# Kernel tuning notes

Hardware: AMD Instinct MI355X
Metric: run time of the kernel (lower is better)

## Reference

```python
import jax, jax.numpy as jnp
import numpy as np

N = 4096
D = 1024  # hidden_size == att_size


def setup_inputs() -> dict:
    key = jax.random.key(0)
    ks = jax.random.split(key, 10)
    s = 0.02
    return {
        "q": jax.random.normal(ks[0], (N, D), jnp.float32),
        "k": jax.random.normal(ks[1], (N, D), jnp.float32),
        "v": jax.random.normal(ks[2], (N, D), jnp.float32),
        "bias": jax.random.normal(ks[3], (N, N), jnp.float32) * s,
        "Wq": jax.random.normal(ks[4], (D, D), jnp.float32) * s,
        "bq": jnp.zeros((D,), jnp.float32),
        "Wk": jax.random.normal(ks[5], (D, D), jnp.float32) * s,
        "bk": jnp.zeros((D,), jnp.float32),
        "Wv": jax.random.normal(ks[6], (D, D), jnp.float32) * s,
        "bv": jnp.zeros((D,), jnp.float32),
    }


def reference(q, k, v, bias, Wq, bq, Wk, bk, Wv, bv):
    d = q.shape[-1]
    scale = d ** (-0.5)
    # QKV projections (nn.Linear: x @ W.T + b)
    qp = (q @ Wq.T + bq) * scale          # [N, D]
    kp = k @ Wk.T + bk                    # [N, D]
    vp = v @ Wv.T + bv                    # [N, D]
    # full N x N attention (single head, pseudo-batch of 1 in the original)
    scores = qp @ kp.T                    # [N, N]
    att = jax.nn.softmax(scores, axis=-1) + bias  # POST-softmax bias add
    # dropout is identity in eval mode; original casts weights to fp32 here
    out = att.astype(jnp.float32) @ vp    # [N, D]
    return out
```

## Files before the change

kernel.cpp:

```cpp
#include <hip/hip_runtime.h>
#include <hip/hip_bf16.h>
#include <stdint.h>

typedef unsigned short u16;
using bf16x8 = __attribute__((ext_vector_type(8))) __bf16;
using f32x4  = __attribute__((ext_vector_type(4))) float;

__device__ __forceinline__ u16 f2bf(float f) {
    union { float f; unsigned u; } a; a.f = f;
    unsigned u = a.u;
    u += 0x7fffu + ((u >> 16) & 1u);
    return (u16)(u >> 16);
}
__device__ __forceinline__ float bf2f(unsigned bits_hi16) {
    union { unsigned u; float f; } a; a.u = bits_hi16; return a.f;
}

__device__ __forceinline__ void gload_lds16(const void* g, void* l) {
    __builtin_amdgcn_global_load_lds(
        (const __attribute__((address_space(1))) void*)g,
        (__attribute__((address_space(3))) void*)l, 16, 0, 0);
}

__device__ __forceinline__ void xcd_swz(int nx, int ny, int& x, int& y, int& z) {
    const int flat = (int)blockIdx.x + nx * ((int)blockIdx.y + ny * (int)blockIdx.z);
    const int cpx = (nx * ny * (int)gridDim.z) >> 3;
    const int s = (flat & 7) * cpx + (flat >> 3);
    x = s % nx;
    const int t = s / nx;
    y = t % ny;
    z = t / ny;
}

__device__ __forceinline__ void gemm_core(const u16* __restrict__ A,
                                          const u16* __restrict__ B,
                                          int lda, int ldb, int kLen,
                                          int bm, int bn,
                                          u16* sA, u16* sB,
                                          f32x4 acc[4][4])
{
    const int tid  = threadIdx.x;
    const int lane = tid & 63;
    const int wm   = (tid >> 7) & 1;
    const int wn   = (tid >> 6) & 1;

    const u16* Ag0 = A + (long)(bm * 128 + (tid >> 2)) * lda + (tid & 3) * 8;
    const u16* Ag1 = Ag0 + (long)64 * lda;
    const u16* Bg0 = B + (long)(bn * 128 + (tid >> 2)) * ldb + (tid & 3) * 8;
    const u16* Bg1 = Bg0 + (long)64 * ldb;
    u16* la = sA + tid * 8;
    u16* lb = sB + tid * 8;

    const int rfo = (wm * 64 + (lane & 15)) * 32 + (lane >> 4) * 8;
    const int rfoB = (wn * 64 + (lane & 15)) * 32 + (lane >> 4) * 8;

    for (int k0 = 0; k0 < kLen; k0 += 64) {
        gload_lds16(Ag0 + k0, la);
        gload_lds16(Ag1 + k0, la + 2048);
        gload_lds16(Bg0 + k0, lb);
        gload_lds16(Bg1 + k0, lb + 2048);
        gload_lds16(Ag0 + k0 + 32, la + 4096);
        gload_lds16(Ag1 + k0 + 32, la + 6144);
        gload_lds16(Bg0 + k0 + 32, lb + 4096);
        gload_lds16(Bg1 + k0 + 32, lb + 6144);
        __syncthreads();
#pragma unroll
        for (int h = 0; h < 2; h++) {
            const u16* ra = sA + h * 4096 + rfo;
            const u16* rb = sB + h * 4096 + rfoB;
            bf16x8 af[4], bfr[4];
#pragma unroll
            for (int i = 0; i < 4; i++) af[i]  = *(const bf16x8*)(ra + i * 512);
#pragma unroll
            for (int i = 0; i < 4; i++) bfr[i] = *(const bf16x8*)(rb + i * 512);
#pragma unroll
            for (int mi = 0; mi < 4; mi++)
#pragma unroll
                for (int ni = 0; ni < 4; ni++)
                    acc[mi][ni] = __builtin_amdgcn_mfma_f32_16x16x32_bf16(
                        af[mi], bfr[ni], acc[mi][ni], 0, 0, 0);
        }
        __syncthreads();
    }
}

__global__ __launch_bounds__(256)
void cast6(const float* __restrict__ q, const float* __restrict__ k,
           const float* __restrict__ v, const float* __restrict__ wq,
           const float* __restrict__ wk, const float* __restrict__ wv,
           u16* __restrict__ qb, u16* __restrict__ kb, u16* __restrict__ vb,
           u16* __restrict__ wqb, u16* __restrict__ wkb, u16* __restrict__ wvb,
           int nqkv, int nw)
{
    const int z = blockIdx.y;
    const float* s; u16* d; int n;
    switch (z) {
        case 0:  s = q;  d = qb;  n = nqkv; break;
        case 1:  s = k;  d = kb;  n = nqkv; break;
        case 2:  s = v;  d = vb;  n = nqkv; break;
        case 3:  s = wq; d = wqb; n = nw;   break;
        case 4:  s = wk; d = wkb; n = nw;   break;
        default: s = wv; d = wvb; n = nw;   break;
    }
    long i = ((long)blockIdx.x * 256 + threadIdx.x) * 8;
    if (i >= n) return;
    float4 a = *(const float4*)(s + i);
    float4 b = *(const float4*)(s + i + 4);
    ushort4 o0, o1;
    o0.x = f2bf(a.x); o0.y = f2bf(a.y); o0.z = f2bf(a.z); o0.w = f2bf(a.w);
    o1.x = f2bf(b.x); o1.y = f2bf(b.y); o1.z = f2bf(b.z); o1.w = f2bf(b.w);
    *(ushort4*)(d + i)     = o0;
    *(ushort4*)(d + i + 4) = o1;
}

__global__ __launch_bounds__(256, 2)
void proj_gemm(const u16* __restrict__ qb, const u16* __restrict__ kb,
               const u16* __restrict__ vb, const u16* __restrict__ wqb,
               const u16* __restrict__ wkb, const u16* __restrict__ wvb,
               const float* __restrict__ bq, const float* __restrict__ bk,
               const float* __restrict__ bv,
               u16* __restrict__ qp, u16* __restrict__ kp, u16* __restrict__ vpT)
{
    __shared__ __align__(16) u16 sA[8192];
    __shared__ __align__(16) u16 sB[8192];
    int bx, by, bz;
    xcd_swz(8, 32, bx, by, bz);
    const int z = bz;
    const u16* A = (z == 0) ? qb : (z == 1) ? kb : vb;
    const u16* B = (z == 0) ? wqb : (z == 1) ? wkb : wvb;
    const float* bias = (z == 0) ? bq : (z == 1) ? bk : bv;
    u16* OUT = (z == 0) ? qp : (z == 1) ? kp : vpT;
    const float scale = (z == 0) ? 0.03125f : 1.0f;

    f32x4 acc[4][4] = {};
    gemm_core(A, B, 1024, 1024, 1024, by, bx, sA, sB, acc);

    const int lane = threadIdx.x & 63;
    const int wm   = (threadIdx.x >> 7) & 1;
    const int wn   = (threadIdx.x >> 6) & 1;
    const int m0 = by * 128 + wm * 64 + ((lane >> 4) << 2);
    const int n0 = bx * 128 + wn * 64 + (lane & 15);
#pragma unroll
    for (int mi = 0; mi < 4; mi++)
#pragma unroll
        for (int ni = 0; ni < 4; ni++) {
            const int gm = m0 + mi * 16;
            const int gn = n0 + ni * 16;
            const float bb = bias[gn];
#pragma unroll
            for (int r = 0; r < 4; r++) {
                float val = (acc[mi][ni][r] + bb) * scale;
                if (z < 2) OUT[(long)(gm + r) * 1024 + gn] = f2bf(val);
                else       OUT[(long)gn * 4096 + gm + r]   = f2bf(val);
            }
        }
}

__global__ __launch_bounds__(256, 2)
void vproj_gemm(const u16* __restrict__ wvb, const u16* __restrict__ vb,
                const float* __restrict__ bv, u16* __restrict__ vpT)
{
    __shared__ __align__(16) u16 sA[8192];
    __shared__ __align__(16) u16 sB[8192];
    f32x4 acc[4][4] = {};
    gemm_core(wvb, vb, 1024, 1024, 1024, blockIdx.y, blockIdx.x, sA, sB, acc);

    const int lane = threadIdx.x & 63;
    const int wm   = (threadIdx.x >> 7) & 1;
    const int wn   = (threadIdx.x >> 6) & 1;
    const int m0 = blockIdx.y * 128 + wm * 64 + ((lane >> 4) << 2);
    const int n0 = blockIdx.x * 128 + wn * 64 + (lane & 15);
#pragma unroll
    for (int mi = 0; mi < 4; mi++)
#pragma unroll
        for (int ni = 0; ni < 4; ni++) {
            const int gm = m0 + mi * 16;
            const int gn = n0 + ni * 16;
#pragma unroll
            for (int r = 0; r < 4; r++)
                vpT[(long)(gm + r) * 4096 + gn] = f2bf(acc[mi][ni][r] + bv[gm + r]);
        }
}

__global__ __launch_bounds__(256, 2)
void score_gemm(const u16* __restrict__ qp, const u16* __restrict__ kp,
                u16* __restrict__ S)
{
    __shared__ __align__(16) u16 sA[8192];
    __shared__ __align__(16) u16 sB[8192];
    f32x4 acc[4][4] = {};
    gemm_core(qp, kp, 1024, 1024, 1024, blockIdx.y, blockIdx.x, sA, sB, acc);

    const int lane = threadIdx.x & 63;
    const int wm   = (threadIdx.x >> 7) & 1;
    const int wn   = (threadIdx.x >> 6) & 1;
    const int m0 = blockIdx.y * 128 + wm * 64 + ((lane >> 4) << 2);
    const int n0 = blockIdx.x * 128 + wn * 64 + (lane & 15);
#pragma unroll
    for (int mi = 0; mi < 4; mi++)
#pragma unroll
        for (int ni = 0; ni < 4; ni++) {
            const int gm = m0 + mi * 16;
            const int gn = n0 + ni * 16;
#pragma unroll
            for (int r = 0; r < 4; r++)
                S[(long)(gm + r) * 4096 + gn] = f2bf(acc[mi][ni][r]);
        }
}

__global__ __launch_bounds__(256)
void softmax_bias(const u16* __restrict__ S, const float* __restrict__ bias,
                  u16* __restrict__ att)
{
    const long row = blockIdx.x;
    const int tid = threadIdx.x;
    const u16* srow = S + row * 4096 + tid * 16;

    float v[16];
    {
        uint4 a = *(const uint4*)(srow);
        uint4 b = *(const uint4*)(srow + 8);
        unsigned w[8] = {a.x, a.y, a.z, a.w, b.x, b.y, b.z, b.w};
#pragma unroll
        for (int i = 0; i < 8; i++) {
            v[2 * i]     = bf2f(w[i] << 16);
            v[2 * i + 1] = bf2f(w[i] & 0xffff0000u);
        }
    }
    float mx = v[0];
#pragma unroll
    for (int i = 1; i < 16; i++) mx = fmaxf(mx, v[i]);
#pragma unroll
    for (int o = 32; o >= 1; o >>= 1) mx = fmaxf(mx, __shfl_xor(mx, o, 64));
    __shared__ float red[8];
    if ((tid & 63) == 0) red[tid >> 6] = mx;
    __syncthreads();
    mx = fmaxf(fmaxf(red[0], red[1]), fmaxf(red[2], red[3]));
    float sum = 0.f;
#pragma unroll
    for (int i = 0; i < 16; i++) { v[i] = __expf(v[i] - mx); sum += v[i]; }
#pragma unroll
    for (int o = 32; o >= 1; o >>= 1) sum += __shfl_xor(sum, o, 64);
    if ((tid & 63) == 0) red[4 + (tid >> 6)] = sum;
    __syncthreads();
    const float inv = 1.0f / (red[4] + red[5] + red[6] + red[7]);

    const float4* brow = (const float4*)(bias + row * 4096 + tid * 16);
    unsigned o[8];
#pragma unroll
    for (int i = 0; i < 4; i++) {
        float4 b = brow[i];
        unsigned lo = f2bf(v[4 * i + 0] * inv + b.x);
        unsigned hi = f2bf(v[4 * i + 1] * inv + b.y);
        o[2 * i] = lo | (hi << 16);
        lo = f2bf(v[4 * i + 2] * inv + b.z);
        hi = f2bf(v[4 * i + 3] * inv + b.w);
        o[2 * i + 1] = lo | (hi << 16);
    }
    u16* arow = att + row * 4096 + tid * 16;
    *(uint4*)(arow)     = make_uint4(o[0], o[1], o[2], o[3]);
    *(uint4*)(arow + 8) = make_uint4(o[4], o[5], o[6], o[7]);
}

__global__ __launch_bounds__(256, 2)
void out_gemm(const u16* __restrict__ att, const u16* __restrict__ vpT,
              float* __restrict__ P)
{
    __shared__ __align__(16) u16 sA[8192];
    __shared__ __align__(16) u16 sB[8192];
    int bx, by, bz;
    xcd_swz(8, 32, bx, by, bz);
    const u16* A = att + bz * 2048;
    const u16* B = vpT + bz * 2048;
    float* O = P + (long)bz * 4096 * 1024;

    f32x4 acc[4][4] = {};
    gemm_core(A, B, 4096, 4096, 2048, by, bx, sA, sB, acc);

    const int lane = threadIdx.x & 63;
    const int wm   = (threadIdx.x >> 7) & 1;
    const int wn   = (threadIdx.x >> 6) & 1;
    const int m0 = by * 128 + wm * 64 + ((lane >> 4) << 2);
    const int n0 = bx * 128 + wn * 64 + (lane & 15);
#pragma unroll
    for (int mi = 0; mi < 4; mi++)
#pragma unroll
        for (int ni = 0; ni < 4; ni++) {
            const int gm = m0 + mi * 16;
            const int gn = n0 + ni * 16;
#pragma unroll
            for (int r = 0; r < 4; r++)
                O[(long)(gm + r) * 1024 + gn] = acc[mi][ni][r];
        }
}

__global__ __launch_bounds__(256)
void addp(const float* __restrict__ P, float* __restrict__ O)
{
    long i = ((long)blockIdx.x * 256 + threadIdx.x) * 4;
    float4 a = *(const float4*)(P + i);
    float4 b = *(const float4*)(P + 4194304 + i);
    float4 r;
    r.x = a.x + b.x; r.y = a.y + b.y; r.z = a.z + b.z; r.w = a.w + b.w;
    *(float4*)(O + i) = r;
}

extern "C" void kernel_launch(void* const* d_in, const int* in_sizes, int n_in,
                              void* d_out, int out_size, void* d_ws, size_t ws_size,
                              hipStream_t stream)
{
    const float* q    = (const float*)d_in[0];
    const float* k    = (const float*)d_in[1];
    const float* v    = (const float*)d_in[2];
    const float* bias = (const float*)d_in[3];
    const float* Wq   = (const float*)d_in[4];
    const float* bq   = (const float*)d_in[5];
    const float* Wk   = (const float*)d_in[6];
    const float* bk   = (const float*)d_in[7];
    const float* Wv   = (const float*)d_in[8];
    const float* bv   = (const float*)d_in[9];
    float* out = (float*)d_out;

    uint8_t* ws = (uint8_t*)d_ws;
    const size_t MB = 1u << 20;
    u16* qb  = (u16*)(ws);
    u16* kb  = (u16*)(ws + 8 * MB);
    u16* vb  = (u16*)(ws + 16 * MB);
    u16* wqb = (u16*)(ws + 24 * MB);
    u16* wkb = (u16*)(ws + 26 * MB);
    u16* wvb = (u16*)(ws + 28 * MB);
    u16* qp  = (u16*)(ws + 30 * MB);
    u16* kp  = (u16*)(ws + 38 * MB);
    u16* vpT = (u16*)(ws + 46 * MB);
    u16* S   = (u16*)(ws + 54 * MB);
    u16* att = (u16*)(ws);
    float* P = (float*)(ws + 86 * MB);

    cast6<<<dim3(2048, 6), 256, 0, stream>>>(q, k, v, Wq, Wk, Wv,
                                             qb, kb, vb, wqb, wkb, wvb,
                                             4096 * 1024, 1024 * 1024);
    proj_gemm<<<dim3(8, 32, 2), 256, 0, stream>>>(qb, kb, vb, wqb, wkb, wvb,
                                                  bq, bk, bv, qp, kp, vpT);
    vproj_gemm<<<dim3(32, 8), 256, 0, stream>>>(wvb, vb, bv, vpT);
    score_gemm<<<dim3(32, 32), 256, 0, stream>>>(qp, kp, S);
    softmax_bias<<<dim3(4096), 256, 0, stream>>>(S, bias, att);
    out_gemm<<<dim3(8, 32, 2), 256, 0, stream>>>(att, vpT, P);
    addp<<<dim3(4096), 256, 0, stream>>>(P, out);
}
```

Before: 303.6 us.

## Add triple-buffered swizzled GEMM core, merge V projection, atomic split-K output

Measured after the change: 330.4 us. 8.8% more time.

```diff
diff --git a/kernel.cpp b/kernel.cpp
--- a/kernel.cpp
+++ b/kernel.cpp
@@ -51,7 +51,7 @@
     u16* la = sA + tid * 8;
     u16* lb = sB + tid * 8;
 
-    const int rfo = (wm * 64 + (lane & 15)) * 32 + (lane >> 4) * 8;
+    const int rfo  = (wm * 64 + (lane & 15)) * 32 + (lane >> 4) * 8;
     const int rfoB = (wn * 64 + (lane & 15)) * 32 + (lane >> 4) * 8;
 
     for (int k0 = 0; k0 < kLen; k0 += 64) {
@@ -84,6 +84,84 @@
     }
 }
 
+__device__ __forceinline__ void gemm128_core(const u16* __restrict__ A,
+                                             const u16* __restrict__ B,
+                                             int lda, int ldb, int T,
+                                             int rowA0, int rowB0,
+                                             u16* lds,
+                                             f32x4 acc[4][4],
+                                             int wm, int wn)
+{
+    const int tid  = (int)threadIdx.x;
+    const int l    = tid & 63;
+
+    const int srcswz = 8 * ((tid & 3) ^ ((tid >> 3) & 3));
+    const u16* pA = A + (long)(rowA0 + (tid >> 2)) * lda + srcswz;
+    const u16* pB = B + (long)(rowB0 + (tid >> 2)) * ldb + srcswz;
+    const long a64 = 64 * (long)lda;
+    const long b64 = 64 * (long)ldb;
+    const int dst = tid * 8;
+
+    const int fsw = 8 * ((l >> 4) ^ ((l >> 1) & 3));
+    const int fA = (wm * 64 + (l & 15)) * 32 + fsw;
+    const int fB = (wn * 64 + (l & 15)) * 32 + fsw;
+
+    f32x4 (&ac)[4][4] = *(f32x4(*)[4][4])acc;
+    bf16x8 af[4], bf[4];
+
+#define STG(tile, bb)                                                          \
+    {                                                                          \
+        const long co = (long)(tile) * 32;                                     \
+        u16* d = lds + (bb) + dst;                                             \
+        gload_lds16(pA + co, d);                                               \
+        gload_lds16(pA + co + a64, d + 2048);                                  \
+        gload_lds16(pB + co, d + 4096);                                        \
+        gload_lds16(pB + co + b64, d + 6144);                                  \
+    }
+#define RD(bb)                                                                 \
+    {                                                                          \
+        const u16* Ar = lds + (bb) + fA;                                       \
+        const u16* Br = lds + (bb) + 4096 + fB;                                \
+        _Pragma("unroll")                                                      \
+        for (int i = 0; i < 4; i++) af[i] = *(const bf16x8*)(Ar + i * 512);    \
+        _Pragma("unroll")                                                      \
+        for (int i = 0; i < 4; i++) bf[i] = *(const bf16x8*)(Br + i * 512);    \
+    }
+
+    STG(0, 0); STG(1, 8192);
+    asm volatile("s_waitcnt vmcnt(4)" ::: "memory");
+    __builtin_amdgcn_s_barrier();
+
+    int cur = 0;
+    int stg = 2;
+    for (int t = 0; t < T; ++t) {
+        const int ts = (t + 2 < T) ? t + 2 : T - 1;
+
+        RD(cur * 8192);
+        STG(ts, stg * 8192);
+        asm volatile("s_waitcnt vmcnt(4)" ::: "memory");
+        __builtin_amdgcn_s_barrier();
+        asm volatile("s_waitcnt lgkmcnt(0)" ::: "memory");
+        __builtin_amdgcn_sched_barrier(0);
+        __builtin_amdgcn_s_setprio(1);
+#pragma unroll
+        for (int mi = 0; mi < 4; mi++)
+#pragma unroll
+            for (int ni = 0; ni < 4; ni++)
+                ac[mi][ni] = __builtin_amdgcn_mfma_f32_16x16x32_bf16(
+                    af[mi], bf[ni], ac[mi][ni], 0, 0, 0);
+        __builtin_amdgcn_s_setprio(0);
+        __builtin_amdgcn_s_barrier();
+
+        cur = (cur == 2) ? 0 : cur + 1;
+        stg = (stg == 2) ? 0 : stg + 1;
+    }
+    asm volatile("s_waitcnt vmcnt(0)" ::: "memory");
+
+#undef STG
+#undef RD
+}
+
 __global__ __launch_bounds__(256)
 void cast6(const float* __restrict__ q, const float* __restrict__ k,
            const float* __restrict__ v, const float* __restrict__ wq,
@@ -113,6 +191,13 @@
     *(ushort4*)(d + i + 4) = o1;
 }
 
+__global__ __launch_bounds__(256)
+void zero_out(float* __restrict__ O)
+{
+    long i = ((long)blockIdx.x * 256 + threadIdx.x) * 4;
+    *(float4*)(O + i) = make_float4(0.f, 0.f, 0.f, 0.f);
+}
+
 __global__ __launch_bounds__(256, 2)
 void proj_gemm(const u16* __restrict__ qb, const u16* __restrict__ kb,
                const u16* __restrict__ vb, const u16* __restrict__ wqb,
@@ -126,18 +211,37 @@
     int bx, by, bz;
     xcd_swz(8, 32, bx, by, bz);
     const int z = bz;
-    const u16* A = (z == 0) ? qb : (z == 1) ? kb : vb;
-    const u16* B = (z == 0) ? wqb : (z == 1) ? wkb : wvb;
-    const float* bias = (z == 0) ? bq : (z == 1) ? bk : bv;
-    u16* OUT = (z == 0) ? qp : (z == 1) ? kp : vpT;
-    const float scale = (z == 0) ? 0.03125f : 1.0f;
 
     f32x4 acc[4][4] = {};
-    gemm_core(A, B, 1024, 1024, 1024, by, bx, sA, sB, acc);
-
     const int lane = threadIdx.x & 63;
     const int wm   = (threadIdx.x >> 7) & 1;
     const int wn   = (threadIdx.x >> 6) & 1;
+
+    if (z == 2) {
+        gemm_core(wvb, vb, 1024, 1024, 1024, bx, by, sA, sB, acc);
+        const int m0 = bx * 128 + wm * 64 + ((lane >> 4) << 2);
+        const int n0 = by * 128 + wn * 64 + (lane & 15);
+#pragma unroll
+        for (int mi = 0; mi < 4; mi++)
+#pragma unroll
+            for (int ni = 0; ni < 4; ni++) {
+                const int gm = m0 + mi * 16;
+                const int gn = n0 + ni * 16;
+#pragma unroll
+                for (int r = 0; r < 4; r++)
+                    vpT[(long)(gm + r) * 4096 + gn] = f2bf(acc[mi][ni][r] + bv[gm + r]);
+            }
+        return;
+    }
+
+    const u16* A = (z == 0) ? qb : kb;
+    const u16* B = (z == 0) ? wqb : wkb;
+    const float* bias = (z == 0) ? bq : bk;
+    u16* OUT = (z == 0) ? qp : kp;
+    const float scale = (z == 0) ? 0.03125f : 1.0f;
+
+    gemm_core(A, B, 1024, 1024, 1024, by, bx, sA, sB, acc);
+
     const int m0 = by * 128 + wm * 64 + ((lane >> 4) << 2);
     const int n0 = bx * 128 + wn * 64 + (lane & 15);
 #pragma unroll
@@ -148,54 +252,29 @@
             const int gn = n0 + ni * 16;
             const float bb = bias[gn];
 #pragma unroll
-            for (int r = 0; r < 4; r++) {
-                float val = (acc[mi][ni][r] + bb) * scale;
-                if (z < 2) OUT[(long)(gm + r) * 1024 + gn] = f2bf(val);
-                else       OUT[(long)gn * 4096 + gm + r]   = f2bf(val);
-            }
+            for (int r = 0; r < 4; r++)
+                OUT[(long)(gm + r) * 1024 + gn] = f2bf((acc[mi][ni][r] + bb) * scale);
         }
 }
 
-__global__ __launch_bounds__(256, 2)
-void vproj_gemm(const u16* __restrict__ wvb, const u16* __restrict__ vb,
-                const float* __restrict__ bv, u16* __restrict__ vpT)
-{
-    __shared__ __align__(16) u16 sA[8192];
-    __shared__ __align__(16) u16 sB[8192];
+__global__ __launch_bounds__(256, 3)
+void score_gemm128(const u16* __restrict__ qp, const u16* __restrict__ kp,
+                   u16* __restrict__ S)
+{
+    __shared__ __align__(16) u16 lds[24576];
+
+    int bx, by, bz;
+    xcd_swz(32, 32, bx, by, bz);
+
+    const int l  = (int)threadIdx.x & 63;
+    const int wm = ((int)threadIdx.x >> 7) & 1;
+    const int wn = ((int)threadIdx.x >> 6) & 1;
+
     f32x4 acc[4][4] = {};
-    gemm_core(wvb, vb, 1024, 1024, 1024, blockIdx.y, blockIdx.x, sA, sB, acc);
-
-    const int lane = threadIdx.x & 63;
-    const int wm   = (threadIdx.x >> 7) & 1;
-    const int wn   = (threadIdx.x >> 6) & 1;
-    const int m0 = blockIdx.y * 128 + wm * 64 + ((lane >> 4) << 2);
-    const int n0 = blockIdx.x * 128 + wn * 64 + (lane & 15);
-#pragma unroll
-    for (int mi = 0; mi < 4; mi++)
-#pragma unroll
-        for (int ni = 0; ni < 4; ni++) {
-            const int gm = m0 + mi * 16;
-            const int gn = n0 + ni * 16;
-#pragma unroll
-            for (int r = 0; r < 4; r++)
-                vpT[(long)(gm + r) * 4096 + gn] = f2bf(acc[mi][ni][r] + bv[gm + r]);
-        }
-}
-
-__global__ __launch_bounds__(256, 2)
-void score_gemm(const u16* __restrict__ qp, const u16* __restrict__ kp,
-                u16* __restrict__ S)
-{
-    __shared__ __align__(16) u16 sA[8192];
-    __shared__ __align__(16) u16 sB[8192];
-    f32x4 acc[4][4] = {};
-    gemm_core(qp, kp, 1024, 1024, 1024, blockIdx.y, blockIdx.x, sA, sB, acc);
-
-    const int lane = threadIdx.x & 63;
-    const int wm   = (threadIdx.x >> 7) & 1;
-    const int wn   = (threadIdx.x >> 6) & 1;
-    const int m0 = blockIdx.y * 128 + wm * 64 + ((lane >> 4) << 2);
-    const int n0 = blockIdx.x * 128 + wn * 64 + (lane & 15);
+    gemm128_core(qp, kp, 1024, 1024, 32, by * 128, bx * 128, lds, acc, wm, wn);
+
+    const int m0 = by * 128 + wm * 64 + ((l >> 4) << 2);
+    const int n0 = bx * 128 + wn * 64 + (l & 15);
 #pragma unroll
     for (int mi = 0; mi < 4; mi++)
 #pragma unroll
@@ -262,26 +341,26 @@
     *(uint4*)(arow + 8) = make_uint4(o[4], o[5], o[6], o[7]);
 }
 
-__global__ __launch_bounds__(256, 2)
-void out_gemm(const u16* __restrict__ att, const u16* __restrict__ vpT,
-              float* __restrict__ P)
-{
-    __shared__ __align__(16) u16 sA[8192];
-    __shared__ __align__(16) u16 sB[8192];
+__global__ __launch_bounds__(256, 3)
+void out_gemm128(const u16* __restrict__ att, const u16* __restrict__ vpT,
+                 float* __restrict__ O)
+{
+    __shared__ __align__(16) u16 lds[24576];
+
     int bx, by, bz;
     xcd_swz(8, 32, bx, by, bz);
-    const u16* A = att + bz * 2048;
-    const u16* B = vpT + bz * 2048;
-    float* O = P + (long)bz * 4096 * 1024;
+    const u16* A = att + bz * 1024;
+    const u16* B = vpT + bz * 1024;
+
+    const int l  = (int)threadIdx.x & 63;
+    const int wm = ((int)threadIdx.x >> 7) & 1;
+    const int wn = ((int)threadIdx.x >> 6) & 1;
 
     f32x4 acc[4][4] = {};
-    gemm_core(A, B, 4096, 4096, 2048, by, bx, sA, sB, acc);
-
-    const int lane = threadIdx.x & 63;
-    const int wm   = (threadIdx.x >> 7) & 1;
-    const int wn   = (threadIdx.x >> 6) & 1;
-    const int m0 = by * 128 + wm * 64 + ((lane >> 4) << 2);
-    const int n0 = bx * 128 + wn * 64 + (lane & 15);
+    gemm128_core(A, B, 4096, 4096, 32, by * 128, bx * 128, lds, acc, wm, wn);
+
+    const int m0 = by * 128 + wm * 64 + ((l >> 4) << 2);
+    const int n0 = bx * 128 + wn * 64 + (l & 15);
 #pragma unroll
     for (int mi = 0; mi < 4; mi++)
 #pragma unroll
@@ -290,19 +369,8 @@
             const int gn = n0 + ni * 16;
 #pragma unroll
             for (int r = 0; r < 4; r++)
-                O[(long)(gm + r) * 1024 + gn] = acc[mi][ni][r];
+                atomicAdd(&O[(long)(gm + r) * 1024 + gn], acc[mi][ni][r]);
         }
-}
-
-__global__ __launch_bounds__(256)
-void addp(const float* __restrict__ P, float* __restrict__ O)
-{
-    long i = ((long)blockIdx.x * 256 + threadIdx.x) * 4;
-    float4 a = *(const float4*)(P + i);
-    float4 b = *(const float4*)(P + 4194304 + i);
-    float4 r;
-    r.x = a.x + b.x; r.y = a.y + b.y; r.z = a.z + b.z; r.w = a.w + b.w;
-    *(float4*)(O + i) = r;
 }
 
 extern "C" void kernel_launch(void* const* d_in, const int* in_sizes, int n_in,
@@ -334,16 +402,14 @@
     u16* vpT = (u16*)(ws + 46 * MB);
     u16* S   = (u16*)(ws + 54 * MB);
     u16* att = (u16*)(ws);
-    float* P = (float*)(ws + 86 * MB);
 
     cast6<<<dim3(2048, 6), 256, 0, stream>>>(q, k, v, Wq, Wk, Wv,
                                              qb, kb, vb, wqb, wkb, wvb,
                                              4096 * 1024, 1024 * 1024);
-    proj_gemm<<<dim3(8, 32, 2), 256, 0, stream>>>(qb, kb, vb, wqb, wkb, wvb,
+    zero_out<<<dim3(4096), 256, 0, stream>>>(out);
+    proj_gemm<<<dim3(8, 32, 3), 256, 0, stream>>>(qb, kb, vb, wqb, wkb, wvb,
                                                   bq, bk, bv, qp, kp, vpT);
-    vproj_gemm<<<dim3(32, 8), 256, 0, stream>>>(wvb, vb, bv, vpT);
-    score_gemm<<<dim3(32, 32), 256, 0, stream>>>(qp, kp, S);
+    score_gemm128<<<dim3(32, 32), 256, 0, stream>>>(qp, kp, S);
     softmax_bias<<<dim3(4096), 256, 0, stream>>>(S, bias, att);
-    out_gemm<<<dim3(8, 32, 2), 256, 0, stream>>>(att, vpT, P);
-    addp<<<dim3(4096), 256, 0, stream>>>(P, out);
-}
+    out_gemm128<<<dim3(8, 32, 4), 256, 0, stream>>>(att, vpT, out);
+}
```
